# Optimization experiments

Hardware: AMD Instinct MI355X
Metric: run time of the kernel (lower is better)

The kernel has to match this reference:

```python
import jax, jax.numpy as jnp
import numpy as np

E = 800000
D = 64
N = 50000

def setup_inputs() -> dict:
    key = jax.random.key(0)
    k1, k2 = jax.random.split(key)
    src = jax.random.normal(k1, (E, D), dtype=jnp.float32)
    index = jax.random.randint(k2, (E,), 0, N, dtype=jnp.int64)
    return {"src": src, "index": index, "dim": 0, "dim_size": N}

def reference(src, index, dim, dim_size):
    # scatter-mean along dim=0: segment sum divided by per-segment counts
    # (torch_scatter mean clamps count to >= 1 so empty segments stay 0).
    sums = jax.ops.segment_sum(src, index, num_segments=dim_size)  # [N, D]
    counts = jax.ops.segment_sum(jnp.ones((src.shape[0],), dtype=src.dtype),
                                 index, num_segments=dim_size)      # [N]
    denom = jnp.maximum(counts, 1.0)
    return sums / denom[:, None]
```

## Files before the change

### kernel.cpp

```cpp
#include <hip/hip_runtime.h>


typedef unsigned int u32;

#define CAP 128
#define OVF_MAX 4096

__global__ void zero_u32_kernel(u32* __restrict__ p, int n) {
    int i = blockIdx.x * blockDim.x + threadIdx.x;
    int stride = gridDim.x * blockDim.x;
    for (; i < n; i += stride) p[i] = 0u;
}

__global__ void slot_scatter_kernel(const int* __restrict__ idx, u32* __restrict__ cnt,
                                    u32* __restrict__ slot, u32* __restrict__ ovf, int E) {
    int i = blockIdx.x * blockDim.x + threadIdx.x;
    int stride = gridDim.x * blockDim.x;
    for (; i < E; i += stride) {
        int n = idx[i];
        u32 pos = atomicAdd(&cnt[n], 1u);
        if (pos < CAP) {
            slot[(long)n * CAP + pos] = (u32)i;
        } else {
            u32 o = atomicAdd(&ovf[0], 1u);
            if (o < OVF_MAX) ovf[1 + o] = (u32)i;
        }
    }
}

__global__ void gather_mean_kernel(const float4* __restrict__ src4, const u32* __restrict__ slot,
                                   const u32* __restrict__ cnt, float4* __restrict__ out4, int N) {
    int seg = blockIdx.x * (blockDim.x >> 6) + (threadIdx.x >> 6);
    if (seg >= N) return;
    int lane = threadIdx.x & 63;
    int g = lane >> 4;
    int q = lane & 15;
    int c = (int)cnt[seg];
    int m = c < CAP ? c : CAP;
    const u32* sl = slot + (long)seg * CAP;
    float4 acc = make_float4(0.f, 0.f, 0.f, 0.f);
    int j = 0;
    while (j < m) {
        int chunk = m - j; if (chunk > 64) chunk = 64;
        u32 myperm = (lane < chunk) ? sl[j + lane] : 0u;
        int k = 0;
        for (; k + 8 <= chunk; k += 8) {
            u32 eA = __shfl(myperm, k + g);
            u32 eB = __shfl(myperm, k + 4 + g);
            float4 vA = src4[(long)eA * 16 + q];
            float4 vB = src4[(long)eB * 16 + q];
            acc.x += vA.x + vB.x; acc.y += vA.y + vB.y;
            acc.z += vA.z + vB.z; acc.w += vA.w + vB.w;
        }
        for (; k < chunk; k += 4) {
            int r = k + g;
            u32 e = __shfl(myperm, r < chunk ? r : k);
            if (r < chunk) {
                float4 v = src4[(long)e * 16 + q];
                acc.x += v.x; acc.y += v.y; acc.z += v.z; acc.w += v.w;
            }
        }
        j += chunk;
    }
    acc.x += __shfl_down(acc.x, 32); acc.y += __shfl_down(acc.y, 32);
    acc.z += __shfl_down(acc.z, 32); acc.w += __shfl_down(acc.w, 32);
    acc.x += __shfl_down(acc.x, 16); acc.y += __shfl_down(acc.y, 16);
    acc.z += __shfl_down(acc.z, 16); acc.w += __shfl_down(acc.w, 16);
    if (g == 0) {
        float inv = 1.0f / (float)(c > 1 ? c : 1);
        acc.x *= inv; acc.y *= inv; acc.z *= inv; acc.w *= inv;
        out4[(long)seg * 16 + q] = acc;
    }
}

__global__ void ovf_fix_kernel(const float* __restrict__ src, const int* __restrict__ idx,
                               const u32* __restrict__ cnt, const u32* __restrict__ ovf,
                               float* __restrict__ out) {
    u32 no = ovf[0]; if (no > OVF_MAX) no = OVF_MAX;
    int nw = (gridDim.x * blockDim.x) >> 6;
    int w  = (blockIdx.x * blockDim.x + threadIdx.x) >> 6;
    int lane = threadIdx.x & 63;
    for (u32 t = (u32)w; t < no; t += (u32)nw) {
        u32 e = ovf[1 + t];
        int n = idx[e];
        u32 c = cnt[n];
        float inv = 1.0f / (float)(c > 1u ? c : 1u);
        atomicAdd(&out[(long)n * 64 + lane], src[(long)e * 64 + lane] * inv);
    }
}

__global__ void zero_f4_kernel(float4* __restrict__ p, long n4) {
    long i = (long)blockIdx.x * blockDim.x + threadIdx.x;
    long stride = (long)gridDim.x * blockDim.x;
    float4 z = make_float4(0.f, 0.f, 0.f, 0.f);
    for (; i < n4; i += stride) p[i] = z;
}
__global__ void scatter_add_kernel(const float4* __restrict__ src4, const int* __restrict__ idx,
                                   float* __restrict__ out, float* __restrict__ cnt, int E) {
    long t = (long)blockIdx.x * blockDim.x + threadIdx.x;
    long total = (long)E * 16;
    long stride = (long)gridDim.x * blockDim.x;
    for (; t < total; t += stride) {
        int e = (int)(t >> 4), c4 = (int)(t & 15);
        int n = idx[e];
        float4 v = src4[(long)e * 16 + c4];
        float* o = out + (long)n * 64 + c4 * 4;
        atomicAdd(o + 0, v.x); atomicAdd(o + 1, v.y);
        atomicAdd(o + 2, v.z); atomicAdd(o + 3, v.w);
        if (c4 == 0) atomicAdd(cnt + n, 1.0f);
    }
}
__global__ void divide_kernel(float4* __restrict__ out4, const float* __restrict__ cnt, int N) {
    long t = (long)blockIdx.x * blockDim.x + threadIdx.x;
    long total = (long)N * 16;
    long stride = (long)gridDim.x * blockDim.x;
    for (; t < total; t += stride) {
        int n = (int)(t >> 4);
        float inv = 1.0f / fmaxf(cnt[n], 1.0f);
        float4 v = out4[t];
        v.x *= inv; v.y *= inv; v.z *= inv; v.w *= inv;
        out4[t] = v;
    }
}

extern "C" void kernel_launch(void* const* d_in, const int* in_sizes, int n_in,
                              void* d_out, int out_size, void* d_ws, size_t ws_size,
                              hipStream_t stream) {
    const float* src = (const float*)d_in[0];
    const int*   idx = (const int*)d_in[1];
    float* out = (float*)d_out;

    const int E = in_sizes[1];
    const int D = in_sizes[0] / E;
    const int N = out_size / D;
    const int BLK = 256;

    const size_t CNT_OFF  = 0;
    const size_t OVF_OFF  = ((size_t)N + 63) & ~63ul;
    const size_t SLOT_OFF = (OVF_OFF + 1 + OVF_MAX + 127) & ~127ul;
    const size_t NEED = (SLOT_OFF + (size_t)N * CAP) * 4;

    if (ws_size >= NEED) {
        u32* W    = (u32*)d_ws;
        u32* cnt  = W + CNT_OFF;
        u32* ovf  = W + OVF_OFF;
        u32* slot = W + SLOT_OFF;

        {
            int span = (int)(OVF_OFF - CNT_OFF) + 1;
            int grid = (span + BLK - 1) / BLK;
            zero_u32_kernel<<<grid, BLK, 0, stream>>>(cnt, span);
        }
        {
            int grid = (E + BLK - 1) / BLK;
            slot_scatter_kernel<<<grid, BLK, 0, stream>>>(idx, cnt, slot, ovf, E);
        }
        {
            int segs_per_blk = BLK / 64;
            int grid = (N + segs_per_blk - 1) / segs_per_blk;
            gather_mean_kernel<<<grid, BLK, 0, stream>>>((const float4*)src, slot, cnt,
                                                         (float4*)out, N);
        }
        {
            ovf_fix_kernel<<<1, 256, 0, stream>>>(src, idx, cnt, ovf, out);
        }
    } else {
        float* cnt = (float*)d_ws;
        {
            long n4 = (long)out_size / 4;
            int grid = (int)((n4 + BLK - 1) / BLK); if (grid > 2048) grid = 2048;
            zero_f4_kernel<<<grid, BLK, 0, stream>>>((float4*)out, n4);
        }
        {
            long n4 = (long)N / 4;
            int grid = (int)((n4 + BLK - 1) / BLK); if (grid > 2048) grid = 2048;
            zero_f4_kernel<<<grid, BLK, 0, stream>>>((float4*)cnt, n4);
        }
        {
            long total = (long)E * 16;
            int grid = (int)((total + BLK - 1) / BLK); if (grid > 2048) grid = 2048;
            scatter_add_kernel<<<grid, BLK, 0, stream>>>((const float4*)src, idx, out, cnt, E);
        }
        {
            long total = (long)N * 16;
            int grid = (int)((total + BLK - 1) / BLK); if (grid > 2048) grid = 2048;
            divide_kernel<<<grid, BLK, 0, stream>>>((float4*)out, cnt, N);
        }
    }
}
```

Before: 352.1 us.

## Fuse zero, slot scatter, gather-mean and overflow fix into one cooperative kernel

Replaces the four-kernel pipeline with a single cooperative kernel that zeroes the counters, bins edge indices into per-segment slots, gathers and averages, then applies overflow corrections. The stages are separated by grid-wide syncs. The gather loop is now persistent and prefetches the next segment's count and slot list. Slot capacity drops from 128 to 32 per segment and the overflow buffer grows, shrinking the slot workspace and its memory traffic. This removes launch gaps and makes the slot table more cache-friendly. The costs are the grid-sync overhead, occupancy limited to what can be co-resident, and more edges routed through the atomic overflow path for heavy segments. The old multi-kernel path is kept as a fallback if the cooperative launch fails.

```diff
diff --git a/kernel.cpp b/kernel.cpp
--- a/kernel.cpp
+++ b/kernel.cpp
@@ -1,10 +1,106 @@
 #include <hip/hip_runtime.h>
+#include <hip/hip_cooperative_groups.h>
+
+namespace cg = cooperative_groups;
 
 
 typedef unsigned int u32;
 
-#define CAP 128
-#define OVF_MAX 4096
+#define CAP 32
+#define OVF_MAX 32768
+
+__global__ __launch_bounds__(256, 4)
+void fused_scatter_mean_kernel(const float4* __restrict__ src4,
+                               const int* __restrict__ idx,
+                               u32* __restrict__ cnt,
+                               u32* __restrict__ ovf,
+                               u32* __restrict__ slot,
+                               float4* __restrict__ out4,
+                               int E, int N)
+{
+    cg::grid_group grid = cg::this_grid();
+    const int tid = blockIdx.x * blockDim.x + threadIdx.x;
+    const int nthreads = gridDim.x * blockDim.x;
+
+    for (int i = tid; i <= N; i += nthreads) {
+        if (i < N) cnt[i] = 0u; else ovf[0] = 0u;
+    }
+    grid.sync();
+
+    for (int i = tid; i < E; i += nthreads) {
+        int n = idx[i];
+        u32 pos = atomicAdd(&cnt[n], 1u);
+        if (pos < CAP) {
+            slot[(long)n * CAP + pos] = (u32)i;
+        } else {
+            u32 o = atomicAdd(&ovf[0], 1u);
+            if (o < OVF_MAX) ovf[1 + o] = (u32)i;
+        }
+    }
+    grid.sync();
+
+    const int lane = threadIdx.x & 63;
+    const int g = lane >> 4;
+    const int q = lane & 15;
+    const int wave = tid >> 6;
+    const int nwaves = nthreads >> 6;
+
+    int s = wave;
+    u32 c = 0, my = 0;
+    if (s < N) {
+        c = cnt[s];
+        my = (lane < CAP) ? slot[(long)s * CAP + lane] : 0u;
+    }
+    while (s < N) {
+        int s2 = s + nwaves;
+        u32 c2 = 0, my2 = 0;
+        if (s2 < N) {
+            c2 = cnt[s2];
+            my2 = (lane < CAP) ? slot[(long)s2 * CAP + lane] : 0u;
+        }
+        int m = (int)(c < CAP ? c : CAP);
+        float4 acc = make_float4(0.f, 0.f, 0.f, 0.f);
+        int k = 0;
+        for (; k + 8 <= m; k += 8) {
+            u32 eA = __shfl(my, k + g);
+            u32 eB = __shfl(my, k + 4 + g);
+            float4 vA = src4[(long)eA * 16 + q];
+            float4 vB = src4[(long)eB * 16 + q];
+            acc.x += vA.x + vB.x; acc.y += vA.y + vB.y;
+            acc.z += vA.z + vB.z; acc.w += vA.w + vB.w;
+        }
+        for (; k < m; k += 4) {
+            int r = k + g;
+            u32 e = __shfl(my, r < m ? r : k);
+            if (r < m) {
+                float4 v = src4[(long)e * 16 + q];
+                acc.x += v.x; acc.y += v.y; acc.z += v.z; acc.w += v.w;
+            }
+        }
+        acc.x += __shfl_down(acc.x, 32); acc.y += __shfl_down(acc.y, 32);
+        acc.z += __shfl_down(acc.z, 32); acc.w += __shfl_down(acc.w, 32);
+        acc.x += __shfl_down(acc.x, 16); acc.y += __shfl_down(acc.y, 16);
+        acc.z += __shfl_down(acc.z, 16); acc.w += __shfl_down(acc.w, 16);
+        if (g == 0) {
+            float inv = 1.0f / (float)(c > 1u ? c : 1u);
+            out4[(long)s * 16 + q] = make_float4(acc.x * inv, acc.y * inv,
+                                                 acc.z * inv, acc.w * inv);
+        }
+        s = s2; c = c2; my = my2;
+    }
+    grid.sync();
+
+    const float* src = (const float*)src4;
+    float* out = (float*)out4;
+    u32 no = ovf[0]; if (no > OVF_MAX) no = OVF_MAX;
+    for (u32 t = (u32)wave; t < no; t += (u32)nwaves) {
+        u32 e = ovf[1 + t];
+        int n = idx[e];
+        u32 cc = cnt[n];
+        float inv = 1.0f / (float)(cc > 1u ? cc : 1u);
+        atomicAdd(&out[(long)n * 64 + lane], src[(long)e * 64 + lane] * inv);
+    }
+}
 
 __global__ void zero_u32_kernel(u32* __restrict__ p, int n) {
     int i = blockIdx.x * blockDim.x + threadIdx.x;
@@ -19,12 +115,8 @@
     for (; i < E; i += stride) {
         int n = idx[i];
         u32 pos = atomicAdd(&cnt[n], 1u);
-        if (pos < CAP) {
-            slot[(long)n * CAP + pos] = (u32)i;
-        } else {
-            u32 o = atomicAdd(&ovf[0], 1u);
-            if (o < OVF_MAX) ovf[1 + o] = (u32)i;
-        }
+        if (pos < CAP) slot[(long)n * CAP + pos] = (u32)i;
+        else { u32 o = atomicAdd(&ovf[0], 1u); if (o < OVF_MAX) ovf[1 + o] = (u32)i; }
     }
 }
 
@@ -33,34 +125,28 @@
     int seg = blockIdx.x * (blockDim.x >> 6) + (threadIdx.x >> 6);
     if (seg >= N) return;
     int lane = threadIdx.x & 63;
-    int g = lane >> 4;
-    int q = lane & 15;
+    int g = lane >> 4, q = lane & 15;
     int c = (int)cnt[seg];
     int m = c < CAP ? c : CAP;
     const u32* sl = slot + (long)seg * CAP;
+    u32 my = (lane < CAP) ? sl[lane] : 0u;
     float4 acc = make_float4(0.f, 0.f, 0.f, 0.f);
-    int j = 0;
-    while (j < m) {
-        int chunk = m - j; if (chunk > 64) chunk = 64;
-        u32 myperm = (lane < chunk) ? sl[j + lane] : 0u;
-        int k = 0;
-        for (; k + 8 <= chunk; k += 8) {
-            u32 eA = __shfl(myperm, k + g);
-            u32 eB = __shfl(myperm, k + 4 + g);
-            float4 vA = src4[(long)eA * 16 + q];
-            float4 vB = src4[(long)eB * 16 + q];
-            acc.x += vA.x + vB.x; acc.y += vA.y + vB.y;
-            acc.z += vA.z + vB.z; acc.w += vA.w + vB.w;
-        }
-        for (; k < chunk; k += 4) {
-            int r = k + g;
-            u32 e = __shfl(myperm, r < chunk ? r : k);
-            if (r < chunk) {
-                float4 v = src4[(long)e * 16 + q];
-                acc.x += v.x; acc.y += v.y; acc.z += v.z; acc.w += v.w;
-            }
-        }
-        j += chunk;
+    int k = 0;
+    for (; k + 8 <= m; k += 8) {
+        u32 eA = __shfl(my, k + g);
+        u32 eB = __shfl(my, k + 4 + g);
+        float4 vA = src4[(long)eA * 16 + q];
+        float4 vB = src4[(long)eB * 16 + q];
+        acc.x += vA.x + vB.x; acc.y += vA.y + vB.y;
+        acc.z += vA.z + vB.z; acc.w += vA.w + vB.w;
+    }
+    for (; k < m; k += 4) {
+        int r = k + g;
+        u32 e = __shfl(my, r < m ? r : k);
+        if (r < m) {
+            float4 v = src4[(long)e * 16 + q];
+            acc.x += v.x; acc.y += v.y; acc.z += v.z; acc.w += v.w;
+        }
     }
     acc.x += __shfl_down(acc.x, 32); acc.y += __shfl_down(acc.y, 32);
     acc.z += __shfl_down(acc.z, 32); acc.w += __shfl_down(acc.w, 32);
@@ -68,8 +154,8 @@
     acc.z += __shfl_down(acc.z, 16); acc.w += __shfl_down(acc.w, 16);
     if (g == 0) {
         float inv = 1.0f / (float)(c > 1 ? c : 1);
-        acc.x *= inv; acc.y *= inv; acc.z *= inv; acc.w *= inv;
-        out4[(long)seg * 16 + q] = acc;
+        out4[(long)seg * 16 + q] = make_float4(acc.x * inv, acc.y * inv,
+                                               acc.z * inv, acc.w * inv);
     }
 }
 
@@ -146,22 +232,40 @@
         u32* ovf  = W + OVF_OFF;
         u32* slot = W + SLOT_OFF;
 
-        {
-            int span = (int)(OVF_OFF - CNT_OFF) + 1;
-            int grid = (span + BLK - 1) / BLK;
-            zero_u32_kernel<<<grid, BLK, 0, stream>>>(cnt, span);
-        }
-        {
-            int grid = (E + BLK - 1) / BLK;
-            slot_scatter_kernel<<<grid, BLK, 0, stream>>>(idx, cnt, slot, ovf, E);
-        }
-        {
-            int segs_per_blk = BLK / 64;
-            int grid = (N + segs_per_blk - 1) / segs_per_blk;
-            gather_mean_kernel<<<grid, BLK, 0, stream>>>((const float4*)src, slot, cnt,
-                                                         (float4*)out, N);
-        }
-        {
+        bool done = false;
+        int maxB = 0;
+        hipError_t rc0 = hipOccupancyMaxActiveBlocksPerMultiprocessor(
+            &maxB, fused_scatter_mean_kernel, BLK, 0);
+        if (rc0 == hipSuccess && maxB > 0) {
+            int grid = maxB * 256;
+            if (grid > 1024) grid = 1024;
+            const float4* src4 = (const float4*)src;
+            float4* out4 = (float4*)out;
+            int E_ = E, N_ = N;
+            void* args[] = { (void*)&src4, (void*)&idx, (void*)&cnt, (void*)&ovf,
+                             (void*)&slot, (void*)&out4, (void*)&E_, (void*)&N_ };
+            hipError_t rc = hipLaunchCooperativeKernel(
+                (const void*)fused_scatter_mean_kernel,
+                dim3(grid), dim3(BLK), args, 0, stream);
+            if (rc == hipSuccess) done = true;
+        }
+
+        if (!done) {
+            {
+                int span = (int)(OVF_OFF - CNT_OFF) + 1;
+                int grid = (span + BLK - 1) / BLK;
+                zero_u32_kernel<<<grid, BLK, 0, stream>>>(cnt, span);
+            }
+            {
+                int grid = (E + BLK - 1) / BLK;
+                slot_scatter_kernel<<<grid, BLK, 0, stream>>>(idx, cnt, slot, ovf, E);
+            }
+            {
+                int segs_per_blk = BLK / 64;
+                int grid = (N + segs_per_blk - 1) / segs_per_blk;
+                gather_mean_kernel<<<grid, BLK, 0, stream>>>((const float4*)src, slot, cnt,
+                                                             (float4*)out, N);
+            }
             ovf_fix_kernel<<<1, 256, 0, stream>>>(src, idx, cnt, ovf, out);
         }
     } else {
```

Result: slower. 653.0 us (+85.4%).
